# Optimization experiments

Hardware: AMD Instinct MI355X
Metric: run time of the kernel (lower is better)

The kernel has to match this reference:

```python
import jax, jax.numpy as jnp
import numpy as np

# Synthetic layered DAG: 8 node-layers of width N -> 7 masked dense layers.
B = 4096        # batch
N = 2048        # nodes per DAG layer (= in_features = out_features)
DEPTH = 7       # number of weight layers (len(L) - 1)
DENSITY = 0.25  # fraction of predecessor edges present (mask sparsity)


def setup_inputs() -> dict:
    key = jax.random.key(0)
    kx, kw, km = jax.random.split(key, 3)
    x = jax.random.normal(kx, (B, N), dtype=jnp.float32)
    # Mask M: [DEPTH, N+1, N]; random 0/1 edges, last row (bias) all ones.
    m = (jax.random.uniform(km, (DEPTH, N + 1, N)) < DENSITY).astype(jnp.float32)
    M = m.at[:, -1, :].set(1.0)
    # Kaiming-uniform per column: bound = 1/sqrt(nnz_j) (torch code's init),
    # nonzero only at masked positions (W initialized to zeros elsewhere).
    nnz = jnp.maximum(M.sum(axis=1, keepdims=True), 1.0)  # [DEPTH,1,N]
    u = jax.random.uniform(kw, (DEPTH, N + 1, N), minval=-1.0, maxval=1.0)
    W = (u / jnp.sqrt(nnz)) * M
    return {"x": x, "W": W, "M": M}


def reference(x, W, M):
    # activations buffer semantics collapse to a per-layer chain because each
    # layer's preds are exactly the previous DAG layer; sinks = last layer.
    def step(acts, wm):
        w, m = wm  # [N+1, N] each
        h = jnp.concatenate(
            [acts, jnp.ones((acts.shape[0], 1), acts.dtype)], axis=1)  # [B, N+1]
        acts = jax.nn.relu(h @ (m * w))  # masked dense matmul + ReLU
        return acts, None

    out, _ = jax.lax.scan(step, x, (W, M))
    return out  # [B, N] activations of sink nodes
```

## Files before the change

### kernel.cpp

```cpp
#include <hip/hip_runtime.h>
#include <hip/hip_bf16.h>

typedef __bf16 bf16_t;
typedef __bf16 v8bf __attribute__((ext_vector_type(8)));
typedef __bf16 v4bf __attribute__((ext_vector_type(4)));
typedef float  v4f  __attribute__((ext_vector_type(4)));

#define B_ROWS 4096
#define N_COLS 2048
#define K_FULL 2049
#define K_PAD  2112
#define DEPTH  7

#define BM 128
#define BN 128
#define BK 64
#define NT (K_PAD / BK)

__global__ __launch_bounds__(256) void wt_kernel(const float* __restrict__ W,
                                                 bf16_t* __restrict__ Wt) {
  __shared__ float t[64][65];
  const int l  = blockIdx.z;
  const int k0 = blockIdx.x * 64;
  const int n0 = blockIdx.y * 64;
  const int tid = threadIdx.x;
  const int r  = tid >> 4;
  const int c4 = (tid & 15) * 4;
  const float* Wl = W + (size_t)l * K_FULL * N_COLS;
#pragma unroll
  for (int it = 0; it < 4; ++it) {
    const int k = k0 + r + it * 16;
    float4 v = make_float4(0.f, 0.f, 0.f, 0.f);
    if (k < K_FULL) v = *(const float4*)&Wl[(size_t)k * N_COLS + n0 + c4];
    t[c4 + 0][r + it * 16] = v.x;
    t[c4 + 1][r + it * 16] = v.y;
    t[c4 + 2][r + it * 16] = v.z;
    t[c4 + 3][r + it * 16] = v.w;
  }
  __syncthreads();
  bf16_t* Wtl = Wt + (size_t)l * N_COLS * K_PAD;
#pragma unroll
  for (int it = 0; it < 4; ++it) {
    const int n = r + it * 16;
    v4bf o;
    o[0] = (bf16_t)t[n][c4 + 0];
    o[1] = (bf16_t)t[n][c4 + 1];
    o[2] = (bf16_t)t[n][c4 + 2];
    o[3] = (bf16_t)t[n][c4 + 3];
    *(v4bf*)&Wtl[(size_t)(n0 + n) * K_PAD + k0 + c4] = o;
  }
}

__global__ __launch_bounds__(256) void init_kernel(const float* __restrict__ x,
                                                   bf16_t* __restrict__ A0,
                                                   bf16_t* __restrict__ A1) {
  const int c4 = (blockIdx.x * 256 + threadIdx.x) * 4;
  const int r  = blockIdx.y;
  if (c4 >= K_PAD) return;
  v4bf o;
  if (c4 < N_COLS) {
    const float4 v = *(const float4*)&x[(size_t)r * N_COLS + c4];
    o[0] = (bf16_t)v.x; o[1] = (bf16_t)v.y; o[2] = (bf16_t)v.z; o[3] = (bf16_t)v.w;
  } else {
    o[0] = (bf16_t)(c4 == N_COLS ? 1.0f : 0.0f);
    o[1] = (bf16_t)0.0f; o[2] = (bf16_t)0.0f; o[3] = (bf16_t)0.0f;
  }
  *(v4bf*)&A0[(size_t)r * K_PAD + c4] = o;
  if (c4 >= N_COLS) *(v4bf*)&A1[(size_t)r * K_PAD + c4] = o;
}

__global__ __launch_bounds__(256, 2) void gemm_kernel(
    const bf16_t* __restrict__ A, const bf16_t* __restrict__ Bt,
    bf16_t* __restrict__ Cn, float* __restrict__ Co) {
  __shared__ __align__(16) bf16_t As[2][BM * BK];
  __shared__ __align__(16) bf16_t Bs[2][BN * BK];

  const int tid  = threadIdx.x;
  const int wave = tid >> 6;
  const int lane = tid & 63;
  const int m0 = blockIdx.y * BM;
  const int n0 = blockIdx.x * BN;
  const int wm = (wave & 1) * 64;
  const int wn = (wave >> 1) * 64;
  const int quad = lane >> 4;
  const int l16  = lane & 15;

  int srow[4], scol[4];
#pragma unroll
  for (int c = 0; c < 4; ++c) {
    const int gran = wave * 256 + c * 64 + lane;
    srow[c] = gran >> 3;
    scol[c] = ((gran & 7) ^ (srow[c] & 7)) << 3;
  }

  const size_t arow_off[4] = {
      (size_t)(m0 + srow[0]) * K_PAD + scol[0],
      (size_t)(m0 + srow[1]) * K_PAD + scol[1],
      (size_t)(m0 + srow[2]) * K_PAD + scol[2],
      (size_t)(m0 + srow[3]) * K_PAD + scol[3]};
  const size_t brow_off[4] = {
      (size_t)(n0 + srow[0]) * K_PAD + scol[0],
      (size_t)(n0 + srow[1]) * K_PAD + scol[1],
      (size_t)(n0 + srow[2]) * K_PAD + scol[2],
      (size_t)(n0 + srow[3]) * K_PAD + scol[3]};

  auto issue = [&](int kt, int buf) {
    const int kbase = kt * BK;
    char* asb = (char*)&As[buf][0] + wave * 4096;
    char* bsb = (char*)&Bs[buf][0] + wave * 4096;
#pragma unroll
    for (int c = 0; c < 4; ++c) {
      __builtin_amdgcn_global_load_lds(
          (const __attribute__((address_space(1))) void*)(A + arow_off[c] + kbase),
          (__attribute__((address_space(3))) void*)(asb + c * 1024), 16, 0, 0);
    }
#pragma unroll
    for (int c = 0; c < 4; ++c) {
      __builtin_amdgcn_global_load_lds(
          (const __attribute__((address_space(1))) void*)(Bt + brow_off[c] + kbase),
          (__attribute__((address_space(3))) void*)(bsb + c * 1024), 16, 0, 0);
    }
  };

  v4f acc[4][4] = {};

  issue(0, 0);
  for (int kt = 0; kt < NT; ++kt) {
    const int cur = kt & 1;
    if (kt + 1 < NT) {
      issue(kt + 1, cur ^ 1);
      asm volatile("s_waitcnt vmcnt(8)" ::: "memory");
    } else {
      asm volatile("s_waitcnt vmcnt(0)" ::: "memory");
    }
    asm volatile("s_barrier" ::: "memory");

    const bf16_t* as = &As[cur][0];
    const bf16_t* bs = &Bs[cur][0];
#pragma unroll
    for (int ks = 0; ks < 2; ++ks) {
      v8bf af[4], bfr[4];
#pragma unroll
      for (int i = 0; i < 4; ++i) {
        const int arow = wm + i * 16 + l16;
        const int kg   = ks * 4 + quad;
        af[i] = *(const v8bf*)&as[arow * BK + ((kg ^ (arow & 7)) << 3)];
        const int brow = wn + i * 16 + l16;
        bfr[i] = *(const v8bf*)&bs[brow * BK + ((kg ^ (brow & 7)) << 3)];
      }
#pragma unroll
      for (int i = 0; i < 4; ++i)
#pragma unroll
        for (int j = 0; j < 4; ++j)
          acc[i][j] = __builtin_amdgcn_mfma_f32_16x16x32_bf16(af[i], bfr[j],
                                                              acc[i][j], 0, 0, 0);
    }
    asm volatile("s_barrier" ::: "memory");
  }

#pragma unroll
  for (int i = 0; i < 4; ++i) {
#pragma unroll
    for (int j = 0; j < 4; ++j) {
#pragma unroll
      for (int r = 0; r < 4; ++r) {
        float v = acc[i][j][r];
        v = v > 0.0f ? v : 0.0f;
        const int row = m0 + wm + i * 16 + quad * 4 + r;
        const int col = n0 + wn + j * 16 + l16;
        if (Co) Co[(size_t)row * N_COLS + col] = v;
        else    Cn[(size_t)row * K_PAD + col] = (bf16_t)v;
      }
    }
  }
}

extern "C" void kernel_launch(void* const* d_in, const int* in_sizes, int n_in,
                              void* d_out, int out_size, void* d_ws, size_t ws_size,
                              hipStream_t stream) {
  const float* x = (const float*)d_in[0];
  const float* W = (const float*)d_in[1];
  float* out = (float*)d_out;

  char* ws = (char*)d_ws;
  const size_t wtBytes = (size_t)DEPTH * N_COLS * K_PAD * sizeof(bf16_t);
  const size_t aBytes  = (size_t)B_ROWS * K_PAD * sizeof(bf16_t);
  bf16_t* Wt = (bf16_t*)ws;
  bf16_t* A0 = (bf16_t*)(ws + wtBytes);
  bf16_t* A1 = (bf16_t*)(ws + wtBytes + aBytes);

  wt_kernel<<<dim3(K_PAD / 64, N_COLS / 64, DEPTH), 256, 0, stream>>>(W, Wt);
  init_kernel<<<dim3((K_PAD / 4 + 255) / 256, B_ROWS), 256, 0, stream>>>(x, A0, A1);

  bf16_t* bufs[2] = {A0, A1};
  for (int l = 0; l < DEPTH; ++l) {
    const bf16_t* Ain = bufs[l & 1];
    bf16_t* Aout      = bufs[(l + 1) & 1];
    const bf16_t* Bl  = Wt + (size_t)l * N_COLS * K_PAD;
    const bool last   = (l == DEPTH - 1);
    gemm_kernel<<<dim3(N_COLS / BN, B_ROWS / BM), 256, 0, stream>>>(
        Ain, Bl, last ? nullptr : Aout, last ? out : nullptr);
  }
}
```

Baseline: 525.0 us.

## Load GEMM B fragments directly into registers instead of staging through LDS

The weight (B) tile no longer goes through shared memory. Each wave now loads its own MFMA B fragments straight from global memory into double-buffered registers, while A stays on the asynchronous global-to-LDS path. The main loop is unrolled by two so the two register buffers alternate, and the old manual vmcnt/barrier handling is replaced by __syncthreads. This removes half of the LDS traffic and footprint, but waves that share the same columns now load B twice from global memory. It also adds about 64 VGPRs per thread, and the B loads are strided 16-byte accesses across rows.

```diff
diff --git a/kernel.cpp b/kernel.cpp
--- a/kernel.cpp
+++ b/kernel.cpp
@@ -73,7 +73,6 @@
     const bf16_t* __restrict__ A, const bf16_t* __restrict__ Bt,
     bf16_t* __restrict__ Cn, float* __restrict__ Co) {
   __shared__ __align__(16) bf16_t As[2][BM * BK];
-  __shared__ __align__(16) bf16_t Bs[2][BN * BK];
 
   const int tid  = threadIdx.x;
   const int wave = tid >> 6;
@@ -92,71 +91,81 @@
     srow[c] = gran >> 3;
     scol[c] = ((gran & 7) ^ (srow[c] & 7)) << 3;
   }
-
-  const size_t arow_off[4] = {
+  const size_t aoff[4] = {
       (size_t)(m0 + srow[0]) * K_PAD + scol[0],
       (size_t)(m0 + srow[1]) * K_PAD + scol[1],
       (size_t)(m0 + srow[2]) * K_PAD + scol[2],
       (size_t)(m0 + srow[3]) * K_PAD + scol[3]};
-  const size_t brow_off[4] = {
-      (size_t)(n0 + srow[0]) * K_PAD + scol[0],
-      (size_t)(n0 + srow[1]) * K_PAD + scol[1],
-      (size_t)(n0 + srow[2]) * K_PAD + scol[2],
-      (size_t)(n0 + srow[3]) * K_PAD + scol[3]};
-
-  auto issue = [&](int kt, int buf) {
+
+  auto issueA = [&](int kt, int buf) {
     const int kbase = kt * BK;
-    char* asb = (char*)&As[buf][0] + wave * 4096;
-    char* bsb = (char*)&Bs[buf][0] + wave * 4096;
+    char* dst = (char*)&As[buf][0] + wave * 4096;
 #pragma unroll
     for (int c = 0; c < 4; ++c) {
       __builtin_amdgcn_global_load_lds(
-          (const __attribute__((address_space(1))) void*)(A + arow_off[c] + kbase),
-          (__attribute__((address_space(3))) void*)(asb + c * 1024), 16, 0, 0);
-    }
-#pragma unroll
-    for (int c = 0; c < 4; ++c) {
-      __builtin_amdgcn_global_load_lds(
-          (const __attribute__((address_space(1))) void*)(Bt + brow_off[c] + kbase),
-          (__attribute__((address_space(3))) void*)(bsb + c * 1024), 16, 0, 0);
+          (const __attribute__((address_space(1))) void*)(A + aoff[c] + kbase),
+          (__attribute__((address_space(3))) void*)(dst + c * 1024), 16, 0, 0);
     }
   };
 
+  const bf16_t* bbase[4][2];
+#pragma unroll
+  for (int j = 0; j < 4; ++j)
+#pragma unroll
+    for (int ks = 0; ks < 2; ++ks)
+      bbase[j][ks] = Bt + (size_t)(n0 + wn + j * 16 + l16) * K_PAD +
+                     ks * 32 + quad * 8;
+
   v4f acc[4][4] = {};
-
-  issue(0, 0);
-  for (int kt = 0; kt < NT; ++kt) {
-    const int cur = kt & 1;
-    if (kt + 1 < NT) {
-      issue(kt + 1, cur ^ 1);
-      asm volatile("s_waitcnt vmcnt(8)" ::: "memory");
-    } else {
-      asm volatile("s_waitcnt vmcnt(0)" ::: "memory");
-    }
-    asm volatile("s_barrier" ::: "memory");
-
-    const bf16_t* as = &As[cur][0];
-    const bf16_t* bs = &Bs[cur][0];
+  v8bf bf0[4][2], bf1[4][2];
+
+  auto loadB = [&](v8bf (&dst)[4][2], int kt) {
+    const int kbase = kt * BK;
+#pragma unroll
+    for (int j = 0; j < 4; ++j)
+#pragma unroll
+      for (int ks = 0; ks < 2; ++ks)
+        dst[j][ks] = *(const v8bf*)(bbase[j][ks] + kbase);
+  };
+
+  auto compute = [&](int buf, const v8bf (&bfr)[4][2]) {
+    const bf16_t* as = &As[buf][0];
 #pragma unroll
     for (int ks = 0; ks < 2; ++ks) {
-      v8bf af[4], bfr[4];
+      v8bf af[4];
 #pragma unroll
       for (int i = 0; i < 4; ++i) {
         const int arow = wm + i * 16 + l16;
         const int kg   = ks * 4 + quad;
         af[i] = *(const v8bf*)&as[arow * BK + ((kg ^ (arow & 7)) << 3)];
-        const int brow = wn + i * 16 + l16;
-        bfr[i] = *(const v8bf*)&bs[brow * BK + ((kg ^ (brow & 7)) << 3)];
       }
 #pragma unroll
       for (int i = 0; i < 4; ++i)
 #pragma unroll
         for (int j = 0; j < 4; ++j)
-          acc[i][j] = __builtin_amdgcn_mfma_f32_16x16x32_bf16(af[i], bfr[j],
+          acc[i][j] = __builtin_amdgcn_mfma_f32_16x16x32_bf16(af[i], bfr[j][ks],
                                                               acc[i][j], 0, 0, 0);
     }
-    asm volatile("s_barrier" ::: "memory");
-  }
+  };
+
+  issueA(0, 0);
+  loadB(bf0, 0);
+  __syncthreads();
+
+  for (int kt = 0; kt < NT - 1; kt += 2) {
+    issueA(kt + 1, (kt + 1) & 1);
+    loadB(bf1, kt + 1);
+    compute(kt & 1, bf0);
+    __syncthreads();
+
+    if (kt + 2 < NT) {
+      issueA(kt + 2, (kt + 2) & 1);
+      loadB(bf0, kt + 2);
+    }
+    compute((kt + 1) & 1, bf1);
+    __syncthreads();
+  }
+  compute((NT - 1) & 1, bf0);
 
 #pragma unroll
   for (int i = 0; i < 4; ++i) {
```

Result: slower. 779.4 us (+48.5%).

## Split GEMM tile across eight waves and drop LDS double buffering

Applied to the files above, without the earlier changes.

Each block now runs 512 threads as eight waves, each computing a 64x32 sub-tile of the same 128x128 output tile instead of 64x64. The double-buffered LDS prefetch pipeline is replaced by a single buffer guarded by two __syncthreads per K step. This halves LDS use and per-wave accumulators to allow higher occupancy under launch bounds (512, 4). In exchange, global loads no longer overlap MFMA work within a block, the tighter register budget risks spills, and the grid only gives about two blocks per CU.

```diff
diff --git a/kernel.cpp b/kernel.cpp
--- a/kernel.cpp
+++ b/kernel.cpp
@@ -69,11 +69,11 @@
   if (c4 >= N_COLS) *(v4bf*)&A1[(size_t)r * K_PAD + c4] = o;
 }
 
-__global__ __launch_bounds__(256, 2) void gemm_kernel(
+__global__ __launch_bounds__(512, 4) void gemm_kernel(
     const bf16_t* __restrict__ A, const bf16_t* __restrict__ Bt,
     bf16_t* __restrict__ Cn, float* __restrict__ Co) {
-  __shared__ __align__(16) bf16_t As[2][BM * BK];
-  __shared__ __align__(16) bf16_t Bs[2][BN * BK];
+  __shared__ __align__(16) bf16_t As[BM * BK];
+  __shared__ __align__(16) bf16_t Bs[BN * BK];
 
   const int tid  = threadIdx.x;
   const int wave = tid >> 6;
@@ -81,87 +81,70 @@
   const int m0 = blockIdx.y * BM;
   const int n0 = blockIdx.x * BN;
   const int wm = (wave & 1) * 64;
-  const int wn = (wave >> 1) * 64;
+  const int wn = (wave >> 1) * 32;
   const int quad = lane >> 4;
   const int l16  = lane & 15;
 
-  int srow[4], scol[4];
+  int srow[2], scol[2];
 #pragma unroll
-  for (int c = 0; c < 4; ++c) {
-    const int gran = wave * 256 + c * 64 + lane;
+  for (int c = 0; c < 2; ++c) {
+    const int gran = wave * 128 + c * 64 + lane;
     srow[c] = gran >> 3;
     scol[c] = ((gran & 7) ^ (srow[c] & 7)) << 3;
   }
+  const size_t aoff[2] = {(size_t)(m0 + srow[0]) * K_PAD + scol[0],
+                          (size_t)(m0 + srow[1]) * K_PAD + scol[1]};
+  const size_t boff[2] = {(size_t)(n0 + srow[0]) * K_PAD + scol[0],
+                          (size_t)(n0 + srow[1]) * K_PAD + scol[1]};
 
-  const size_t arow_off[4] = {
-      (size_t)(m0 + srow[0]) * K_PAD + scol[0],
-      (size_t)(m0 + srow[1]) * K_PAD + scol[1],
-      (size_t)(m0 + srow[2]) * K_PAD + scol[2],
-      (size_t)(m0 + srow[3]) * K_PAD + scol[3]};
-  const size_t brow_off[4] = {
-      (size_t)(n0 + srow[0]) * K_PAD + scol[0],
-      (size_t)(n0 + srow[1]) * K_PAD + scol[1],
-      (size_t)(n0 + srow[2]) * K_PAD + scol[2],
-      (size_t)(n0 + srow[3]) * K_PAD + scol[3]};
+  v4f acc[4][2] = {};
 
-  auto issue = [&](int kt, int buf) {
+  for (int kt = 0; kt < NT; ++kt) {
     const int kbase = kt * BK;
-    char* asb = (char*)&As[buf][0] + wave * 4096;
-    char* bsb = (char*)&Bs[buf][0] + wave * 4096;
+    __syncthreads();
 #pragma unroll
-    for (int c = 0; c < 4; ++c) {
+    for (int c = 0; c < 2; ++c) {
       __builtin_amdgcn_global_load_lds(
-          (const __attribute__((address_space(1))) void*)(A + arow_off[c] + kbase),
-          (__attribute__((address_space(3))) void*)(asb + c * 1024), 16, 0, 0);
+          (const __attribute__((address_space(1))) void*)(A + aoff[c] + kbase),
+          (__attribute__((address_space(3))) void*)((char*)As + wave * 2048 + c * 1024),
+          16, 0, 0);
     }
 #pragma unroll
-    for (int c = 0; c < 4; ++c) {
+    for (int c = 0; c < 2; ++c) {
       __builtin_amdgcn_global_load_lds(
-          (const __attribute__((address_space(1))) void*)(Bt + brow_off[c] + kbase),
-          (__attribute__((address_space(3))) void*)(bsb + c * 1024), 16, 0, 0);
+          (const __attribute__((address_space(1))) void*)(Bt + boff[c] + kbase),
+          (__attribute__((address_space(3))) void*)((char*)Bs + wave * 2048 + c * 1024),
+          16, 0, 0);
     }
-  };
+    __syncthreads();
 
-  v4f acc[4][4] = {};
-
-  issue(0, 0);
-  for (int kt = 0; kt < NT; ++kt) {
-    const int cur = kt & 1;
-    if (kt + 1 < NT) {
-      issue(kt + 1, cur ^ 1);
-      asm volatile("s_waitcnt vmcnt(8)" ::: "memory");
-    } else {
-      asm volatile("s_waitcnt vmcnt(0)" ::: "memory");
-    }
-    asm volatile("s_barrier" ::: "memory");
-
-    const bf16_t* as = &As[cur][0];
-    const bf16_t* bs = &Bs[cur][0];
 #pragma unroll
     for (int ks = 0; ks < 2; ++ks) {
-      v8bf af[4], bfr[4];
+      v8bf af[4], bfr[2];
+      const int kg = ks * 4 + quad;
 #pragma unroll
       for (int i = 0; i < 4; ++i) {
         const int arow = wm + i * 16 + l16;
-        const int kg   = ks * 4 + quad;
-        af[i] = *(const v8bf*)&as[arow * BK + ((kg ^ (arow & 7)) << 3)];
-        const int brow = wn + i * 16 + l16;
-        bfr[i] = *(const v8bf*)&bs[brow * BK + ((kg ^ (brow & 7)) << 3)];
+        af[i] = *(const v8bf*)&As[arow * BK + ((kg ^ (arow & 7)) << 3)];
+      }
+#pragma unroll
+      for (int j = 0; j < 2; ++j) {
+        const int brow = wn + j * 16 + l16;
+        bfr[j] = *(const v8bf*)&Bs[brow * BK + ((kg ^ (brow & 7)) << 3)];
       }
 #pragma unroll
       for (int i = 0; i < 4; ++i)
 #pragma unroll
-        for (int j = 0; j < 4; ++j)
+        for (int j = 0; j < 2; ++j)
           acc[i][j] = __builtin_amdgcn_mfma_f32_16x16x32_bf16(af[i], bfr[j],
                                                               acc[i][j], 0, 0, 0);
     }
-    asm volatile("s_barrier" ::: "memory");
   }
 
 #pragma unroll
   for (int i = 0; i < 4; ++i) {
 #pragma unroll
-    for (int j = 0; j < 4; ++j) {
+    for (int j = 0; j < 2; ++j) {
 #pragma unroll
       for (int r = 0; r < 4; ++r) {
         float v = acc[i][j][r];
@@ -198,7 +181,7 @@
     bf16_t* Aout      = bufs[(l + 1) & 1];
     const bf16_t* Bl  = Wt + (size_t)l * N_COLS * K_PAD;
     const bool last   = (l == DEPTH - 1);
-    gemm_kernel<<<dim3(N_COLS / BN, B_ROWS / BM), 256, 0, stream>>>(
+    gemm_kernel<<<dim3(N_COLS / BN, B_ROWS / BM), 512, 0, stream>>>(
         Ain, Bl, last ? nullptr : Aout, last ? out : nullptr);
   }
 }
```

Result: no change. 517.7 us (-1.4%).
